# Optimization experiments

Hardware: AMD Instinct MI355X
Metric: run time of the kernel (lower is better)

The kernel has to match this reference:

```python
import jax, jax.numpy as jnp
import numpy as np

D_MODEL = 256
N_LAYERS = 2
EXPAND = 2
D_INNER = EXPAND * D_MODEL  # 512
D_STATE = 16
D_CONV = 4
DT_RANK = max(1, D_MODEL // 16)  # 16


def _selective_scan(x, dt, B, C, A, D):
    # x, dt: [b, l, d]   B, C: [b, l, n]   A: [d, n]   D: [d]
    dA = jnp.exp(jnp.einsum('bld,dn->bldn', dt, A))          # discretized state matrix
    dBx = jnp.einsum('bld,bln,bld->bldn', dt, B, x)           # dt * B * u

    def step(h, inp):
        dA_t, dBx_t, C_t = inp                                 # [b,d,n],[b,d,n],[b,n]
        h = dA_t * h + dBx_t
        y = jnp.einsum('bdn,bn->bd', h, C_t)
        return h, y

    h0 = jnp.zeros((x.shape[0], A.shape[0], A.shape[1]), x.dtype)
    _, ys = jax.lax.scan(step, h0, (jnp.moveaxis(dA, 1, 0),
                                    jnp.moveaxis(dBx, 1, 0),
                                    jnp.moveaxis(C, 1, 0)))
    return jnp.moveaxis(ys, 0, 1) + x * D                      # [b, l, d]


def _mamba_block(z, in_w, conv_w, conv_b, xp_w, dt_w, dt_b, A_log, Dp, out_w):
    b, l, _ = z.shape
    xz = z @ in_w.T                                            # [b, l, 2*d_inner]
    x, gate = jnp.split(xz, 2, axis=-1)
    # causal depthwise conv1d over time
    xt = jnp.transpose(x, (0, 2, 1))                            # [b, d_inner, l]
    xt = jax.lax.conv_general_dilated(
        xt, conv_w[:, None, :], window_strides=(1,),
        padding=[(D_CONV - 1, 0)], feature_group_count=D_INNER)
    x = jax.nn.silu(jnp.transpose(xt, (0, 2, 1)) + conv_b)      # [b, l, d_inner]
    x_dbl = x @ xp_w.T                                          # [b, l, dt_rank + 2*d_state]
    dt, Bm, Cm = jnp.split(x_dbl, [DT_RANK, DT_RANK + D_STATE], axis=-1)
    dt = jax.nn.softplus(dt @ dt_w.T + dt_b)                    # [b, l, d_inner]
    A = -jnp.exp(A_log)                                         # [d_inner, d_state]
    y = _selective_scan(x, dt, Bm, Cm, A, Dp)
    y = y * jax.nn.silu(gate)
    return y @ out_w.T                                          # [b, l, d_model]


def setup_inputs() -> dict:
    key = jax.random.key(0)
    ks = jax.random.split(key, 9)
    B, L = 2, 4096
    z = jax.random.normal(ks[0], (B, L, D_MODEL), jnp.float32)
    s = 0.02
    in_proj_w = jax.random.normal(ks[1], (N_LAYERS, 2 * D_INNER, D_MODEL), jnp.float32) * s
    conv_w = jax.random.normal(ks[2], (N_LAYERS, D_INNER, D_CONV), jnp.float32) * 0.2
    conv_b = jnp.zeros((N_LAYERS, D_INNER), jnp.float32)
    x_proj_w = jax.random.normal(ks[3], (N_LAYERS, DT_RANK + 2 * D_STATE, D_INNER), jnp.float32) * s
    dt_proj_w = jax.random.normal(ks[4], (N_LAYERS, D_INNER, DT_RANK), jnp.float32) * 0.1
    dt_proj_b = jax.random.uniform(ks[5], (N_LAYERS, D_INNER), jnp.float32, -4.0, -2.0)
    A_log = jnp.log(jnp.broadcast_to(jnp.arange(1, D_STATE + 1, dtype=jnp.float32),
                                     (N_LAYERS, D_INNER, D_STATE)))
    D_param = jnp.ones((N_LAYERS, D_INNER), jnp.float32)
    out_proj_w = jax.random.normal(ks[6], (N_LAYERS, D_MODEL, D_INNER), jnp.float32) * s
    return {"z": z, "in_proj_w": in_proj_w, "conv_w": conv_w, "conv_b": conv_b,
            "x_proj_w": x_proj_w, "dt_proj_w": dt_proj_w, "dt_proj_b": dt_proj_b,
            "A_log": A_log, "D_param": D_param, "out_proj_w": out_proj_w}


def reference(z, in_proj_w, conv_w, conv_b, x_proj_w, dt_proj_w, dt_proj_b,
              A_log, D_param, out_proj_w):
    for i in range(N_LAYERS):
        z = _mamba_block(z, in_proj_w[i], conv_w[i], conv_b[i], x_proj_w[i],
                         dt_proj_w[i], dt_proj_b[i], A_log[i], D_param[i], out_proj_w[i])
    return z
```

## Files before the change

### kernel.cpp

```cpp
#include <hip/hip_runtime.h>
#include <hip/hip_bf16.h>
#include <cstdint>
#include <cstddef>

#define DM   256
#define DI   512
#define DS   16
#define LSEQ 4096
#define BATCH 2
#define BLROWS (BATCH * LSEQ)
#define NCH  256
#define CLEN 16
#define NSC  16
#define XCP  520

typedef __bf16 bf16x8 __attribute__((ext_vector_type(8)));
typedef float  f32x4  __attribute__((ext_vector_type(4)));
typedef unsigned short u16;
typedef u16 u16x8 __attribute__((ext_vector_type(8)));

__device__ __forceinline__ u16 f2bfu(float f) {
    union { float f; unsigned u; } c; c.f = f;
    unsigned u = c.u;
    return (u16)((u + 0x7fffu + ((u >> 16) & 1u)) >> 16);
}
__device__ __forceinline__ float bfu2f(u16 u) {
    union { unsigned u; float f; } c; c.u = ((unsigned)u) << 16; return c.f;
}
__device__ __forceinline__ float siluf(float v) {
    return v * (1.0f / (1.0f + __expf(-v)));
}
__device__ __forceinline__ void gload_lds16(const void* g, void* l) {
    __builtin_amdgcn_global_load_lds(
        (const __attribute__((address_space(1))) unsigned int*)g,
        (__attribute__((address_space(3))) unsigned int*)l, 16, 0, 0);
}

#define POW_TREE(an, e1)                                                     \
    {   float e2 = (e1)*(e1), e4 = e2*e2, e8 = e4*e4;                        \
        an[0]=(e1); an[1]=e2; an[2]=e2*(e1); an[3]=e4; an[4]=e4*(e1);        \
        an[5]=e4*e2; an[6]=e4*an[2]; an[7]=e8; an[8]=e8*(e1); an[9]=e8*e2;   \
        an[10]=e8*an[2]; an[11]=e8*e4; an[12]=e8*an[4]; an[13]=e8*an[5];     \
        an[14]=e8*an[6]; an[15]=e8*e8; }

#define N_INW  (2*1024*256)
#define N_OUTW (2*256*512)
#define N_XPW  (2*64*512)
#define N_Z    (BLROWS*DM)
__global__ __launch_bounds__(256) void cast_all_k(
    const float* __restrict__ in_w, const float* __restrict__ out_w,
    const float* __restrict__ xp_w, const float* __restrict__ z,
    u16* __restrict__ inw_bf, u16* __restrict__ outw_bf,
    u16* __restrict__ xpw_bf, u16* __restrict__ z_bf) {
    int i = blockIdx.x * 256 + threadIdx.x;
    if (i < N_INW) {
        inw_bf[i] = f2bfu(in_w[i]);
    } else if (i < N_INW + N_OUTW) {
        int j = i - N_INW;
        outw_bf[j] = f2bfu(out_w[j]);
    } else if (i < N_INW + N_OUTW + N_XPW) {
        int j = i - (N_INW + N_OUTW);
        int k = j & 511, o = (j >> 9) & 63, l = j >> 15;
        xpw_bf[j] = f2bfu((o < 48) ? xp_w[(l * 48 + o) * 512 + k] : 0.0f);
    } else {
        int j = i - (N_INW + N_OUTW + N_XPW);
        z_bf[j] = f2bfu(z[j]);
    }
}

__global__ __launch_bounds__(256) void gemm_in_k(
    const __bf16* __restrict__ A, const __bf16* __restrict__ B,
    u16* __restrict__ Cb, int M, int N, int K) {
    __shared__ __bf16 As[128 * 32];
    __shared__ __bf16 Bs[128 * 32];
    int tid = threadIdx.x, wave = tid >> 6, lane = tid & 63;
    int bm = blockIdx.x * 128, bn = blockIdx.y * 128;
    int wm = (wave & 1) * 64, wn = (wave >> 1) * 64;
    int row = lane & 15, q = lane >> 4;
    int srow = lane >> 2, sseg = lane & 3;
    f32x4 acc[4][4] = {};
    for (int k0 = 0; k0 < K; k0 += 32) {
        #pragma unroll
        for (int i = 0; i < 2; ++i) {
            int r0 = wave * 32 + i * 16;
            gload_lds16(A + (size_t)(bm + r0 + srow) * K + k0 + sseg * 8, As + r0 * 32);
            gload_lds16(B + (size_t)(bn + r0 + srow) * K + k0 + sseg * 8, Bs + r0 * 32);
        }
        __syncthreads();
        bf16x8 af[4], bfr[4];
        #pragma unroll
        for (int mi = 0; mi < 4; ++mi)
            af[mi] = *(const bf16x8*)&As[(wm + mi*16 + row) * 32 + q * 8];
        #pragma unroll
        for (int ni = 0; ni < 4; ++ni)
            bfr[ni] = *(const bf16x8*)&Bs[(wn + ni*16 + row) * 32 + q * 8];
        #pragma unroll
        for (int mi = 0; mi < 4; ++mi)
            #pragma unroll
            for (int ni = 0; ni < 4; ++ni)
                acc[mi][ni] = __builtin_amdgcn_mfma_f32_16x16x32_bf16(
                    af[mi], bfr[ni], acc[mi][ni], 0, 0, 0);
        __syncthreads();
    }
    #pragma unroll
    for (int mi = 0; mi < 4; ++mi)
        #pragma unroll
        for (int r = 0; r < 4; ++r) {
            size_t gr = (size_t)(bm + wm + mi*16 + q*4 + r) * N;
            #pragma unroll
            for (int ni = 0; ni < 4; ++ni)
                Cb[gr + bn + wn + ni*16 + row] = f2bfu(acc[mi][ni][r]);
        }
}

__global__ __launch_bounds__(512, 6) void fused_a_k(
    const u16* __restrict__ xz, const float* __restrict__ cw,
    const float* __restrict__ cb, const __bf16* __restrict__ xpw,
    const float* __restrict__ dtw, const float* __restrict__ dtb,
    const float* __restrict__ Alog,
    u16* __restrict__ xcb, u16* __restrict__ dtob,
    float* __restrict__ BCg, u16* __restrict__ Pb, u16* __restrict__ Sb) {
    __shared__ u16 xc_s[CLEN * XCP];
    __shared__ float xd_h[2][CLEN * 68];
    int tid = threadIdx.x;
    int c = blockIdx.x, b = blockIdx.y;
    int flat = b * NCH + c;
    int bl0 = b * LSEQ + c * CLEN;
    int d = tid;

    {
        float w0 = cw[d*4], w1 = cw[d*4+1], w2 = cw[d*4+2], w3 = cw[d*4+3];
        float bias = cb[d];
        float xm3 = 0.f, xm2 = 0.f, xm1 = 0.f;
        int l0 = c * CLEN;
        if (l0 - 3 >= 0) xm3 = bfu2f(xz[(size_t)(bl0 - 3) * 1024 + d]);
        if (l0 - 2 >= 0) xm2 = bfu2f(xz[(size_t)(bl0 - 2) * 1024 + d]);
        if (l0 - 1 >= 0) xm1 = bfu2f(xz[(size_t)(bl0 - 1) * 1024 + d]);
        #pragma unroll 4
        for (int t = 0; t < CLEN; ++t) {
            float xcur = bfu2f(xz[(size_t)(bl0 + t) * 1024 + d]);
            float acc = fmaf(w0, xm3, fmaf(w1, xm2, fmaf(w2, xm1, fmaf(w3, xcur, bias))));
            float v = siluf(acc);
            u16 vb = f2bfu(v);
            xc_s[t * XCP + d] = vb;
            xcb[(size_t)(bl0 + t) * DI + d] = vb;
            xm3 = xm2; xm2 = xm1; xm1 = xcur;
        }
    }
    __syncthreads();

    {
        int wave = tid >> 6, lane = tid & 63;
        int row = lane & 15, q = lane >> 4;
        int nt = wave & 3, kh = wave >> 2;
        f32x4 acc = {0.f, 0.f, 0.f, 0.f};
        #pragma unroll
        for (int kb = 0; kb < 8; ++kb) {
            int kk = (kh*8 + kb) * 32;
            bf16x8 a = *(const bf16x8*)&xc_s[row * XCP + kk + q*8];
            bf16x8 bb = *(const bf16x8*)(xpw + (size_t)(nt*16 + row) * 512 + kk + q*8);
            acc = __builtin_amdgcn_mfma_f32_16x16x32_bf16(a, bb, acc, 0, 0, 0);
        }
        #pragma unroll
        for (int r = 0; r < 4; ++r)
            xd_h[kh][(q*4 + r) * 68 + nt*16 + row] = acc[r];
    }
    __syncthreads();
    for (int j = tid; j < CLEN * 68; j += 512) xd_h[0][j] += xd_h[1][j];
    __syncthreads();

    {
        int t = tid >> 5, cc = tid & 31;
        BCg[(size_t)flat * (CLEN*32) + tid] = xd_h[0][t*68 + 16 + cc];
    }

    {
        float dtwr[16];
        const f32x4* w4 = (const f32x4*)(dtw + (size_t)d * 16);
        #pragma unroll
        for (int g = 0; g < 4; ++g) { f32x4 v = w4[g];
            dtwr[g*4] = v[0]; dtwr[g*4+1] = v[1]; dtwr[g*4+2] = v[2]; dtwr[g*4+3] = v[3]; }
        float dtbv = dtb[d];
        float Ac0; bool fastp = true;
        {
            const f32x4* a4 = (const f32x4*)(Alog + (size_t)d * 16);
            f32x4 v0 = a4[0];
            Ac0 = -__expf(v0[0]);
            #pragma unroll
            for (int g = 0; g < 4; ++g) { f32x4 v = a4[g];
                #pragma unroll
                for (int j = 0; j < 4; ++j) { int n = g*4 + j; if (n) {
                    float acn = -__expf(v[j]);
                    fastp = fastp && (fabsf(acn - (float)(n+1)*Ac0) <= 1e-4f*fabsf(acn));
                } } }
        }
        float s[16];
        #pragma unroll
        for (int n = 0; n < 16; ++n) s[n] = 0.f;
        float Sdt = 0.f;
        if (fastp) {
            for (int t = 0; t < CLEN; ++t) {
                float acc = dtbv;
                #pragma unroll
                for (int r = 0; r < 16; ++r) acc = fmaf(xd_h[0][t*68 + r], dtwr[r], acc);
                float dtraw = (acc > 20.0f) ? acc : logf(1.0f + __expf(acc));
                u16 dtu = f2bfu(dtraw);
                dtob[(size_t)(bl0 + t) * DI + d] = dtu;
                float dtv = bfu2f(dtu);
                float xv = bfu2f(xc_s[t * XCP + d]);
                float dx = dtv * xv;
                Sdt += dtv;
                float e1 = __expf(dtv * Ac0);
                float an[16];
                POW_TREE(an, e1)
                #pragma unroll
                for (int n = 0; n < 16; ++n)
                    s[n] = fmaf(an[n], s[n], xd_h[0][t*68 + 16 + n] * dx);
            }
        } else {
            for (int t = 0; t < CLEN; ++t) {
                float acc = dtbv;
                #pragma unroll
                for (int r = 0; r < 16; ++r) acc = fmaf(xd_h[0][t*68 + r], dtwr[r], acc);
                float dtraw = (acc > 20.0f) ? acc : logf(1.0f + __expf(acc));
                u16 dtu = f2bfu(dtraw);
                dtob[(size_t)(bl0 + t) * DI + d] = dtu;
                float dtv = bfu2f(dtu);
                float xv = bfu2f(xc_s[t * XCP + d]);
                float dx = dtv * xv;
                Sdt += dtv;
                #pragma unroll
                for (int n = 0; n < 16; ++n) {
                    float an = __expf(dtv * -__expf(Alog[(size_t)d*16 + n]));
                    s[n] = fmaf(an, s[n], xd_h[0][t*68 + 16 + n] * dx);
                }
            }
        }
        float pw[16];
        if (fastp) {
            float E1 = __expf(Ac0 * Sdt);
            POW_TREE(pw, E1)
        } else {
            #pragma unroll
            for (int n = 0; n < 16; ++n)
                pw[n] = __expf(-__expf(Alog[(size_t)d*16 + n]) * Sdt);
        }
        size_t base = ((size_t)flat * DI + d) * 16;
        u16x8 pv0, pv1, sv0, sv1;
        #pragma unroll
        for (int n = 0; n < 8; ++n) {
            pv0[n] = f2bfu(pw[n]);  pv1[n] = f2bfu(pw[8+n]);
            sv0[n] = f2bfu(s[n]);   sv1[n] = f2bfu(s[8+n]);
        }
        *(u16x8*)(Pb + base)     = pv0;  *(u16x8*)(Pb + base + 8) = pv1;
        *(u16x8*)(Sb + base)     = sv0;  *(u16x8*)(Sb + base + 8) = sv1;
    }
}

__global__ __launch_bounds__(256) void scan1_k(
    const u16* __restrict__ Pb, const u16* __restrict__ Sb,
    float* __restrict__ Pagg, float* __restrict__ Sagg) {
    int gid = blockIdx.x * 256 + threadIdx.x;
    int scg = gid >> 13, elow = gid & 8191;
    int b = scg >> 4, sc = scg & 15;
    int cbase = b * NCH + sc * 16;
    float h = 0.f, p = 1.f;
    #pragma unroll
    for (int k = 0; k < 16; ++k) {
        size_t a = (size_t)(cbase + k) * 8192 + elow;
        float Pv = bfu2f(Pb[a]), Sv = bfu2f(Sb[a]);
        h = fmaf(Pv, h, Sv);
        p *= Pv;
    }
    Pagg[(size_t)scg * 8192 + elow] = p;
    Sagg[(size_t)scg * 8192 + elow] = h;
}

__global__ __launch_bounds__(256) void scan2_k(
    const u16* __restrict__ Pb, const u16* __restrict__ Sb,
    const float* __restrict__ Pagg, const float* __restrict__ Sagg,
    u16* __restrict__ Hg) {
    int gid = blockIdx.x * 256 + threadIdx.x;
    int scg = gid >> 13, elow = gid & 8191;
    int b = scg >> 4, sc = scg & 15;
    int cbase = b * NCH + sc * 16;
    float h = 0.f;
    for (int s2 = 0; s2 < sc; ++s2) {
        size_t ai = (size_t)(b*16 + s2) * 8192 + elow;
        h = fmaf(Pagg[ai], h, Sagg[ai]);
    }
    #pragma unroll
    for (int k = 0; k < 16; ++k) {
        size_t a = (size_t)(cbase + k) * 8192 + elow;
        Hg[a] = f2bfu(h);
        h = fmaf(bfu2f(Pb[a]), h, bfu2f(Sb[a]));
    }
}

__global__ __launch_bounds__(512, 6) void fused_c_k(
    const u16* __restrict__ xcb, const u16* __restrict__ dtob,
    const float* __restrict__ BCg, const u16* __restrict__ Hg,
    const float* __restrict__ Alog, const float* __restrict__ Dp,
    const u16* __restrict__ xz, const __bf16* __restrict__ outw,
    u16* __restrict__ Ob, float* __restrict__ Of) {
    __shared__ u16 y_s[CLEN * XCP];
    __shared__ float BCs[CLEN * 32];
    int tid = threadIdx.x;
    int c = blockIdx.x, b = blockIdx.y;
    int flat = b * NCH + c;
    int bl0 = b * LSEQ + c * CLEN;
    int d = tid;

    BCs[tid] = BCg[(size_t)flat * (CLEN*32) + tid];

    float Ac0; bool fastp = true;
    {
        const f32x4* a4 = (const f32x4*)(Alog + (size_t)d * 16);
        f32x4 v0 = a4[0];
        Ac0 = -__expf(v0[0]);
        #pragma unroll
        for (int g = 0; g < 4; ++g) { f32x4 v = a4[g];
            #pragma unroll
            for (int j = 0; j < 4; ++j) { int n = g*4 + j; if (n) {
                float acn = -__expf(v[j]);
                fastp = fastp && (fabsf(acn - (float)(n+1)*Ac0) <= 1e-4f*fabsf(acn));
            } } }
    }
    float h[16];
    {
        const u16* h8 = Hg + ((size_t)flat * DI + d) * 16;
        u16x8 hv0 = *(const u16x8*)h8;
        u16x8 hv1 = *(const u16x8*)(h8 + 8);
        #pragma unroll
        for (int n = 0; n < 8; ++n) { h[n] = bfu2f(hv0[n]); h[8+n] = bfu2f(hv1[n]); }
    }
    float Dv = Dp[d];
    __syncthreads();

    if (fastp) {
        for (int t = 0; t < CLEN; ++t) {
            float dtv = bfu2f(dtob[(size_t)(bl0 + t) * DI + d]);
            float xv  = bfu2f(xcb[(size_t)(bl0 + t) * DI + d]);
            float gv  = bfu2f(xz[(size_t)(bl0 + t) * 1024 + DI + d]);
            float dx = dtv * xv;
            float e1 = __expf(dtv * Ac0);
            float an[16];
            POW_TREE(an, e1)
            float y0 = 0.f, y1 = 0.f, y2 = 0.f, y3 = 0.f;
            #pragma unroll
            for (int n = 0; n < 4; ++n) {
                h[n]    = fmaf(an[n],    h[n],    BCs[t*32 + n]    * dx);
                h[4+n]  = fmaf(an[4+n],  h[4+n],  BCs[t*32 + 4+n]  * dx);
                h[8+n]  = fmaf(an[8+n],  h[8+n],  BCs[t*32 + 8+n]  * dx);
                h[12+n] = fmaf(an[12+n], h[12+n], BCs[t*32 + 12+n] * dx);
                y0 = fmaf(h[n],    BCs[t*32 + 16 + n],    y0);
                y1 = fmaf(h[4+n],  BCs[t*32 + 16 + 4+n],  y1);
                y2 = fmaf(h[8+n],  BCs[t*32 + 16 + 8+n],  y2);
                y3 = fmaf(h[12+n], BCs[t*32 + 16 + 12+n], y3);
            }
            float y = (y0 + y1) + (y2 + y3);
            float yv = fmaf(xv, Dv, y) * siluf(gv);
            y_s[t * XCP + d] = f2bfu(yv);
        }
    } else {
        for (int t = 0; t < CLEN; ++t) {
            float dtv = bfu2f(dtob[(size_t)(bl0 + t) * DI + d]);
            float xv  = bfu2f(xcb[(size_t)(bl0 + t) * DI + d]);
            float gv  = bfu2f(xz[(size_t)(bl0 + t) * 1024 + DI + d]);
            float dx = dtv * xv;
            float y = 0.f;
            #pragma unroll
            for (int n = 0; n < 16; ++n) {
                float an = __expf(dtv * -__expf(Alog[(size_t)d*16 + n]));
                h[n] = fmaf(an, h[n], BCs[t*32 + n] * dx);
                y = fmaf(h[n], BCs[t*32 + 16 + n], y);
            }
            float yv = fmaf(xv, Dv, y) * siluf(gv);
            y_s[t * XCP + d] = f2bfu(yv);
        }
    }
    __syncthreads();

    {
        int wave = tid >> 6, lane = tid & 63;
        int row = lane & 15, q = lane >> 4;
        f32x4 acc[2] = {};
        #pragma unroll
        for (int kb = 0; kb < 16; ++kb) {
            bf16x8 a = *(const bf16x8*)&y_s[row * XCP + kb*32 + q*8];
            #pragma unroll
            for (int ni = 0; ni < 2; ++ni) {
                bf16x8 bb = *(const bf16x8*)(outw +
                    (size_t)(wave*32 + ni*16 + row) * 512 + kb*32 + q*8);
                acc[ni] = __builtin_amdgcn_mfma_f32_16x16x32_bf16(a, bb, acc[ni], 0, 0, 0);
            }
        }
        #pragma unroll
        for (int r = 0; r < 4; ++r) {
            size_t gr = (size_t)(bl0 + q*4 + r) * DM;
            #pragma unroll
            for (int ni = 0; ni < 2; ++ni) {
                int gc = wave*32 + ni*16 + row;
                if (Ob) Ob[gr + gc] = f2bfu(acc[ni][r]);
                else    Of[gr + gc] = acc[ni][r];
            }
        }
    }
}

extern "C" void kernel_launch(void* const* d_in, const int* in_sizes, int n_in,
                              void* d_out, int out_size, void* d_ws, size_t ws_size,
                              hipStream_t stream) {
    (void)in_sizes; (void)n_in; (void)out_size; (void)ws_size;
    const float* z_in   = (const float*)d_in[0];
    const float* in_w   = (const float*)d_in[1];
    const float* conv_w = (const float*)d_in[2];
    const float* conv_b = (const float*)d_in[3];
    const float* xp_w   = (const float*)d_in[4];
    const float* dt_w   = (const float*)d_in[5];
    const float* dt_b   = (const float*)d_in[6];
    const float* A_log  = (const float*)d_in[7];
    const float* D_par  = (const float*)d_in[8];
    const float* out_w  = (const float*)d_in[9];
    float* outp = (float*)d_out;

    char* p = (char*)d_ws;
    auto alloc = [&](size_t bytes) { char* r = p; p += (bytes + 255) & ~(size_t)255; return r; };
    u16* z_bf    = (u16*)alloc((size_t)BLROWS*DM*2);
    u16* z2_bf   = (u16*)alloc((size_t)BLROWS*DM*2);
    u16* xz_bf   = (u16*)alloc((size_t)BLROWS*1024*2);
    u16* xc_bf   = (u16*)alloc((size_t)BLROWS*DI*2);
    u16* dt_bf   = (u16*)alloc((size_t)BLROWS*DI*2);
    u16* inw_bf  = (u16*)alloc((size_t)2*1024*256*2);
    u16* outw_bf = (u16*)alloc((size_t)2*256*512*2);
    u16* xpw_bf  = (u16*)alloc((size_t)2*64*512*2);
    float* BCg   = (float*)alloc((size_t)BATCH*NCH*CLEN*32*4);
    u16* Pbuf    = (u16*)alloc((size_t)BATCH*NCH*DI*DS*2);
    u16* Sbuf    = (u16*)alloc((size_t)BATCH*NCH*DI*DS*2);
    u16* Hbuf    = (u16*)alloc((size_t)BATCH*NCH*DI*DS*2);
    float* PaggG = (float*)alloc((size_t)BATCH*NSC*8192*4);
    float* SaggG = (float*)alloc((size_t)BATCH*NSC*8192*4);

    cast_all_k<<<(N_INW + N_OUTW + N_XPW + N_Z)/256, 256, 0, stream>>>(
        in_w, out_w, xp_w, z_in, inw_bf, outw_bf, xpw_bf, z_bf);

    const u16* zcur = z_bf;
    for (int l = 0; l < 2; ++l) {
        gemm_in_k<<<dim3(BLROWS/128, 1024/128), 256, 0, stream>>>(
            (const __bf16*)zcur, (const __bf16*)(inw_bf + (size_t)l*1024*256),
            xz_bf, BLROWS, 1024, 256);
        fused_a_k<<<dim3(NCH, BATCH), 512, 0, stream>>>(
            xz_bf, conv_w + (size_t)l*DI*4, conv_b + (size_t)l*DI,
            (const __bf16*)(xpw_bf + (size_t)l*64*512),
            dt_w + (size_t)l*DI*16, dt_b + (size_t)l*DI,
            A_log + (size_t)l*DI*DS,
            xc_bf, dt_bf, BCg, Pbuf, Sbuf);
        scan1_k<<<BATCH*NSC*8192/256, 256, 0, stream>>>(Pbuf, Sbuf, PaggG, SaggG);
        scan2_k<<<BATCH*NSC*8192/256, 256, 0, stream>>>(Pbuf, Sbuf, PaggG, SaggG, Hbuf);
        fused_c_k<<<dim3(NCH, BATCH), 512, 0, stream>>>(
            xc_bf, dt_bf, BCg, Hbuf,
            A_log + (size_t)l*DI*DS, D_par + (size_t)l*DI,
            xz_bf, (const __bf16*)(outw_bf + (size_t)l*256*512),
            (l == 0) ? z2_bf : nullptr, (l == 1) ? outp : nullptr);
        zcur = z2_bf;
    }
}
```

Measured before the change: 234.0 us.

## Fuse chunk-scan kernels into output kernel with software grid barriers

Replaces the two separate inter-chunk scan kernels and the output kernel with one persistent kernel that runs both scan phases, separated by atomic grid-wide barriers, before the per-chunk output pass. It also packs dt and conv output into one 32-bit buffer so the final pass does one load instead of two. The aim is to remove two kernel launches and their tail gaps. The barrier needs all 512 blocks to be resident at once, which launch_bounds(512,4) is meant to ensure. It also adds spin-wait cost and a timeout break that could silently produce wrong results.

```diff
diff --git a/kernel.cpp b/kernel.cpp
--- a/kernel.cpp
+++ b/kernel.cpp
@@ -13,10 +13,12 @@
 #define CLEN 16
 #define NSC  16
 #define XCP  520
+#define NBLK 512
 
 typedef __bf16 bf16x8 __attribute__((ext_vector_type(8)));
 typedef float  f32x4  __attribute__((ext_vector_type(4)));
 typedef unsigned short u16;
+typedef unsigned int u32;
 typedef u16 u16x8 __attribute__((ext_vector_type(8)));
 
 __device__ __forceinline__ u16 f2bfu(float f) {
@@ -34,6 +36,22 @@
     __builtin_amdgcn_global_load_lds(
         (const __attribute__((address_space(1))) unsigned int*)g,
         (__attribute__((address_space(3))) unsigned int*)l, 16, 0, 0);
+}
+
+__device__ __forceinline__ void gridbar(int* bar) {
+    __syncthreads();
+    if (threadIdx.x == 0) {
+        __threadfence();
+        atomicAdd(bar, 1);
+        int it = 0;
+        while (__hip_atomic_load(bar, __ATOMIC_RELAXED,
+                                 __HIP_MEMORY_SCOPE_AGENT) < NBLK) {
+            __builtin_amdgcn_s_sleep(8);
+            if (++it > (1 << 22)) break;
+        }
+        __threadfence();
+    }
+    __syncthreads();
 }
 
 #define POW_TREE(an, e1)                                                     \
@@ -51,7 +69,9 @@
     const float* __restrict__ in_w, const float* __restrict__ out_w,
     const float* __restrict__ xp_w, const float* __restrict__ z,
     u16* __restrict__ inw_bf, u16* __restrict__ outw_bf,
-    u16* __restrict__ xpw_bf, u16* __restrict__ z_bf) {
+    u16* __restrict__ xpw_bf, u16* __restrict__ z_bf,
+    int* __restrict__ bars) {
+    if (blockIdx.x == 0 && threadIdx.x < 16) bars[threadIdx.x] = 0;
     int i = blockIdx.x * 256 + threadIdx.x;
     if (i < N_INW) {
         inw_bf[i] = f2bfu(in_w[i]);
@@ -118,8 +138,8 @@
     const float* __restrict__ cb, const __bf16* __restrict__ xpw,
     const float* __restrict__ dtw, const float* __restrict__ dtb,
     const float* __restrict__ Alog,
-    u16* __restrict__ xcb, u16* __restrict__ dtob,
-    float* __restrict__ BCg, u16* __restrict__ Pb, u16* __restrict__ Sb) {
+    u32* __restrict__ dxc, float* __restrict__ BCg,
+    u16* __restrict__ Pb, u16* __restrict__ Sb) {
     __shared__ u16 xc_s[CLEN * XCP];
     __shared__ float xd_h[2][CLEN * 68];
     int tid = threadIdx.x;
@@ -128,6 +148,7 @@
     int bl0 = b * LSEQ + c * CLEN;
     int d = tid;
 
+    u16 vb[CLEN];
     {
         float w0 = cw[d*4], w1 = cw[d*4+1], w2 = cw[d*4+2], w3 = cw[d*4+3];
         float bias = cb[d];
@@ -140,10 +161,8 @@
         for (int t = 0; t < CLEN; ++t) {
             float xcur = bfu2f(xz[(size_t)(bl0 + t) * 1024 + d]);
             float acc = fmaf(w0, xm3, fmaf(w1, xm2, fmaf(w2, xm1, fmaf(w3, xcur, bias))));
-            float v = siluf(acc);
-            u16 vb = f2bfu(v);
-            xc_s[t * XCP + d] = vb;
-            xcb[(size_t)(bl0 + t) * DI + d] = vb;
+            vb[t] = f2bfu(siluf(acc));
+            xc_s[t * XCP + d] = vb[t];
             xm3 = xm2; xm2 = xm1; xm1 = xcur;
         }
     }
@@ -205,9 +224,9 @@
                 for (int r = 0; r < 16; ++r) acc = fmaf(xd_h[0][t*68 + r], dtwr[r], acc);
                 float dtraw = (acc > 20.0f) ? acc : logf(1.0f + __expf(acc));
                 u16 dtu = f2bfu(dtraw);
-                dtob[(size_t)(bl0 + t) * DI + d] = dtu;
+                dxc[(size_t)(bl0 + t) * DI + d] = ((u32)dtu << 16) | (u32)vb[t];
                 float dtv = bfu2f(dtu);
-                float xv = bfu2f(xc_s[t * XCP + d]);
+                float xv = bfu2f(vb[t]);
                 float dx = dtv * xv;
                 Sdt += dtv;
                 float e1 = __expf(dtv * Ac0);
@@ -224,9 +243,9 @@
                 for (int r = 0; r < 16; ++r) acc = fmaf(xd_h[0][t*68 + r], dtwr[r], acc);
                 float dtraw = (acc > 20.0f) ? acc : logf(1.0f + __expf(acc));
                 u16 dtu = f2bfu(dtraw);
-                dtob[(size_t)(bl0 + t) * DI + d] = dtu;
+                dxc[(size_t)(bl0 + t) * DI + d] = ((u32)dtu << 16) | (u32)vb[t];
                 float dtv = bfu2f(dtu);
-                float xv = bfu2f(xc_s[t * XCP + d]);
+                float xv = bfu2f(vb[t]);
                 float dx = dtv * xv;
                 Sdt += dtv;
                 #pragma unroll
@@ -257,51 +276,14 @@
     }
 }
 
-__global__ __launch_bounds__(256) void scan1_k(
+__global__ __launch_bounds__(512, 4) void fused_cs_k(
     const u16* __restrict__ Pb, const u16* __restrict__ Sb,
-    float* __restrict__ Pagg, float* __restrict__ Sagg) {
-    int gid = blockIdx.x * 256 + threadIdx.x;
-    int scg = gid >> 13, elow = gid & 8191;
-    int b = scg >> 4, sc = scg & 15;
-    int cbase = b * NCH + sc * 16;
-    float h = 0.f, p = 1.f;
-    #pragma unroll
-    for (int k = 0; k < 16; ++k) {
-        size_t a = (size_t)(cbase + k) * 8192 + elow;
-        float Pv = bfu2f(Pb[a]), Sv = bfu2f(Sb[a]);
-        h = fmaf(Pv, h, Sv);
-        p *= Pv;
-    }
-    Pagg[(size_t)scg * 8192 + elow] = p;
-    Sagg[(size_t)scg * 8192 + elow] = h;
-}
-
-__global__ __launch_bounds__(256) void scan2_k(
-    const u16* __restrict__ Pb, const u16* __restrict__ Sb,
-    const float* __restrict__ Pagg, const float* __restrict__ Sagg,
-    u16* __restrict__ Hg) {
-    int gid = blockIdx.x * 256 + threadIdx.x;
-    int scg = gid >> 13, elow = gid & 8191;
-    int b = scg >> 4, sc = scg & 15;
-    int cbase = b * NCH + sc * 16;
-    float h = 0.f;
-    for (int s2 = 0; s2 < sc; ++s2) {
-        size_t ai = (size_t)(b*16 + s2) * 8192 + elow;
-        h = fmaf(Pagg[ai], h, Sagg[ai]);
-    }
-    #pragma unroll
-    for (int k = 0; k < 16; ++k) {
-        size_t a = (size_t)(cbase + k) * 8192 + elow;
-        Hg[a] = f2bfu(h);
-        h = fmaf(bfu2f(Pb[a]), h, bfu2f(Sb[a]));
-    }
-}
-
-__global__ __launch_bounds__(512, 6) void fused_c_k(
-    const u16* __restrict__ xcb, const u16* __restrict__ dtob,
-    const float* __restrict__ BCg, const u16* __restrict__ Hg,
+    float* __restrict__ Pagg, float* __restrict__ Sagg,
+    u16* __restrict__ Hg,
+    const u32* __restrict__ dxc, const float* __restrict__ BCg,
     const float* __restrict__ Alog, const float* __restrict__ Dp,
     const u16* __restrict__ xz, const __bf16* __restrict__ outw,
+    int* __restrict__ bars,
     u16* __restrict__ Ob, float* __restrict__ Of) {
     __shared__ u16 y_s[CLEN * XCP];
     __shared__ float BCs[CLEN * 32];
@@ -326,6 +308,46 @@
                 fastp = fastp && (fabsf(acn - (float)(n+1)*Ac0) <= 1e-4f*fabsf(acn));
             } } }
     }
+    float Dv = Dp[d];
+
+    int gid = flat * 512 + tid;
+    int b2 = gid >> 17;
+    int rem = gid & 131071;
+    int sc = rem >> 13, elow = rem & 8191;
+    int cbase = b2 * NCH + sc * 16;
+    float Pr[16], Sr[16];
+    {
+        float h2 = 0.f, pp = 1.f;
+        #pragma unroll
+        for (int k = 0; k < 16; ++k) {
+            size_t a = (size_t)(cbase + k) * 8192 + elow;
+            Pr[k] = bfu2f(Pb[a]); Sr[k] = bfu2f(Sb[a]);
+            h2 = fmaf(Pr[k], h2, Sr[k]);
+            pp *= Pr[k];
+        }
+        size_t ai = (size_t)(b2*NSC + sc) * 8192 + elow;
+        Pagg[ai] = pp;
+        Sagg[ai] = h2;
+    }
+
+    gridbar(&bars[0]);
+
+    {
+        float hs = 0.f;
+        for (int s2 = 0; s2 < sc; ++s2) {
+            size_t ai = (size_t)(b2*NSC + s2) * 8192 + elow;
+            hs = fmaf(Pagg[ai], hs, Sagg[ai]);
+        }
+        #pragma unroll
+        for (int k = 0; k < 16; ++k) {
+            size_t a = (size_t)(cbase + k) * 8192 + elow;
+            Hg[a] = f2bfu(hs);
+            hs = fmaf(Pr[k], hs, Sr[k]);
+        }
+    }
+
+    gridbar(&bars[1]);
+
     float h[16];
     {
         const u16* h8 = Hg + ((size_t)flat * DI + d) * 16;
@@ -334,13 +356,12 @@
         #pragma unroll
         for (int n = 0; n < 8; ++n) { h[n] = bfu2f(hv0[n]); h[8+n] = bfu2f(hv1[n]); }
     }
-    float Dv = Dp[d];
-    __syncthreads();
 
     if (fastp) {
         for (int t = 0; t < CLEN; ++t) {
-            float dtv = bfu2f(dtob[(size_t)(bl0 + t) * DI + d]);
-            float xv  = bfu2f(xcb[(size_t)(bl0 + t) * DI + d]);
+            u32 dxv = dxc[(size_t)(bl0 + t) * DI + d];
+            float dtv = bfu2f((u16)(dxv >> 16));
+            float xv  = bfu2f((u16)(dxv & 0xffffu));
             float gv  = bfu2f(xz[(size_t)(bl0 + t) * 1024 + DI + d]);
             float dx = dtv * xv;
             float e1 = __expf(dtv * Ac0);
@@ -364,8 +385,9 @@
         }
     } else {
         for (int t = 0; t < CLEN; ++t) {
-            float dtv = bfu2f(dtob[(size_t)(bl0 + t) * DI + d]);
-            float xv  = bfu2f(xcb[(size_t)(bl0 + t) * DI + d]);
+            u32 dxv = dxc[(size_t)(bl0 + t) * DI + d];
+            float dtv = bfu2f((u16)(dxv >> 16));
+            float xv  = bfu2f((u16)(dxv & 0xffffu));
             float gv  = bfu2f(xz[(size_t)(bl0 + t) * 1024 + DI + d]);
             float dx = dtv * xv;
             float y = 0.f;
@@ -429,8 +451,7 @@
     u16* z_bf    = (u16*)alloc((size_t)BLROWS*DM*2);
     u16* z2_bf   = (u16*)alloc((size_t)BLROWS*DM*2);
     u16* xz_bf   = (u16*)alloc((size_t)BLROWS*1024*2);
-    u16* xc_bf   = (u16*)alloc((size_t)BLROWS*DI*2);
-    u16* dt_bf   = (u16*)alloc((size_t)BLROWS*DI*2);
+    u32* dxc_bf  = (u32*)alloc((size_t)BLROWS*DI*4);
     u16* inw_bf  = (u16*)alloc((size_t)2*1024*256*2);
     u16* outw_bf = (u16*)alloc((size_t)2*256*512*2);
     u16* xpw_bf  = (u16*)alloc((size_t)2*64*512*2);
@@ -440,9 +461,10 @@
     u16* Hbuf    = (u16*)alloc((size_t)BATCH*NCH*DI*DS*2);
     float* PaggG = (float*)alloc((size_t)BATCH*NSC*8192*4);
     float* SaggG = (float*)alloc((size_t)BATCH*NSC*8192*4);
+    int* bars    = (int*)alloc(64);
 
     cast_all_k<<<(N_INW + N_OUTW + N_XPW + N_Z)/256, 256, 0, stream>>>(
-        in_w, out_w, xp_w, z_in, inw_bf, outw_bf, xpw_bf, z_bf);
+        in_w, out_w, xp_w, z_in, inw_bf, outw_bf, xpw_bf, z_bf, bars);
 
     const u16* zcur = z_bf;
     for (int l = 0; l < 2; ++l) {
@@ -454,13 +476,13 @@
             (const __bf16*)(xpw_bf + (size_t)l*64*512),
             dt_w + (size_t)l*DI*16, dt_b + (size_t)l*DI,
             A_log + (size_t)l*DI*DS,
-            xc_bf, dt_bf, BCg, Pbuf, Sbuf);
-        scan1_k<<<BATCH*NSC*8192/256, 256, 0, stream>>>(Pbuf, Sbuf, PaggG, SaggG);
-        scan2_k<<<BATCH*NSC*8192/256, 256, 0, stream>>>(Pbuf, Sbuf, PaggG, SaggG, Hbuf);
-        fused_c_k<<<dim3(NCH, BATCH), 512, 0, stream>>>(
-            xc_bf, dt_bf, BCg, Hbuf,
+            dxc_bf, BCg, Pbuf, Sbuf);
+        fused_cs_k<<<dim3(NCH, BATCH), 512, 0, stream>>>(
+            Pbuf, Sbuf, PaggG, SaggG, Hbuf,
+            dxc_bf, BCg,
             A_log + (size_t)l*DI*DS, D_par + (size_t)l*DI,
             xz_bf, (const __bf16*)(outw_bf + (size_t)l*256*512),
+            bars + (size_t)l*2,
             (l == 0) ? z2_bf : nullptr, (l == 1) ? outp : nullptr);
         zcur = z2_bf;
     }
```

New measurement: 508.7 us. 117% more time.
